# Kernel tuning notes

Hardware: AMD Instinct MI355X
Metric: run time of the kernel (lower is better)

The kernel has to match this reference:

```python
import jax, jax.numpy as jnp
import numpy as np

N_NODES = 20000
N_EDGES = 160000
N_GRAPHS = 100
IN_CH = 64
EDGE_DIM = 8
NEG_SLOPE = 0.2


def _gatv2(x, edge_index, edge_attr, Wl, Wr, We, att, b, heads, ch, n_nodes):
    # GATv2Conv: e_ij = att . leaky_relu(Wl x_j + Wr x_i [+ We e_ij]), softmax over dst i,
    # out_i = sum_j alpha_ij * (Wl x_j), concat heads, + bias.
    src, dst = edge_index[0], edge_index[1]
    xl = (x @ Wl).reshape(-1, heads, ch)  # [N,H,C] source-side transform
    xr = (x @ Wr).reshape(-1, heads, ch)  # [N,H,C] target-side transform
    m = xl[src] + xr[dst]                 # [E,H,C]
    if edge_attr is not None:
        m = m + (edge_attr @ We).reshape(-1, heads, ch)
    m = jax.nn.leaky_relu(m, NEG_SLOPE)
    logit = jnp.einsum('ehc,hc->eh', m, att)                     # [E,H]
    mx = jax.ops.segment_max(logit, dst, num_segments=n_nodes)   # [N,H]
    ex = jnp.exp(logit - mx[dst])
    den = jax.ops.segment_sum(ex, dst, num_segments=n_nodes)     # [N,H]
    alpha = ex / (den[dst] + 1e-16)                              # [E,H]
    out = jax.ops.segment_sum(alpha[:, :, None] * xl[src], dst, num_segments=n_nodes)
    return out.reshape(-1, heads * ch) + b


def setup_inputs() -> dict:
    key = jax.random.key(0)
    ks = jax.random.split(key, 24)
    def rn(k, shape, fan_in):
        return jax.random.normal(k, shape, dtype=jnp.float32) / np.sqrt(fan_in)
    inp = {}
    inp['x'] = jax.random.normal(ks[0], (N_NODES, IN_CH), dtype=jnp.float32)
    inp['edge_attr'] = jax.random.uniform(ks[1], (N_EDGES, EDGE_DIM), dtype=jnp.float32)
    inp['Wl1'] = rn(ks[2], (IN_CH, 1024), IN_CH)
    inp['Wr1'] = rn(ks[3], (IN_CH, 1024), IN_CH)
    inp['We1'] = rn(ks[4], (EDGE_DIM, 1024), EDGE_DIM)
    inp['att1'] = rn(ks[5], (4, 256), 256)
    inp['b1'] = jnp.zeros((1024,), jnp.float32)
    inp['Wl2'] = rn(ks[6], (1024, 256), 1024)
    inp['Wr2'] = rn(ks[7], (1024, 256), 1024)
    inp['We2'] = rn(ks[8], (EDGE_DIM, 256), EDGE_DIM)
    inp['att2'] = rn(ks[9], (4, 64), 64)
    inp['b2'] = jnp.zeros((256,), jnp.float32)
    inp['Wlp'] = rn(ks[10], (256, 384), 256)
    inp['Wrp'] = rn(ks[11], (256, 384), 256)
    inp['attp'] = rn(ks[12], (6, 64), 64)
    inp['bp'] = jnp.zeros((384,), jnp.float32)
    inp['Wfc1'] = rn(ks[13], (384, 64), 384)
    inp['bfc1'] = jnp.zeros((64,), jnp.float32)
    inp['Wfc2'] = rn(ks[14], (64, 1), 64)
    inp['bfc2'] = jnp.zeros((1,), jnp.float32)
    inp['edge_index'] = jax.random.randint(ks[15], (2, N_EDGES), 0, N_NODES, dtype=jnp.int32)
    inp['edge_index_master'] = jax.random.randint(ks[16], (2, N_EDGES), 0, N_NODES, dtype=jnp.int32)
    inp['n_nodes'] = jnp.full((N_GRAPHS,), N_NODES // N_GRAPHS, dtype=jnp.int32)
    return inp


def reference(x, edge_attr, Wl1, Wr1, We1, att1, b1, Wl2, Wr2, We2, att2, b2,
              Wlp, Wrp, attp, bp, Wfc1, bfc1, Wfc2, bfc2,
              edge_index, edge_index_master, n_nodes):
    h = _gatv2(x, edge_index, edge_attr, Wl1, Wr1, We1, att1, b1, 4, 256, N_NODES)
    h = jax.nn.relu(h)
    h = _gatv2(h, edge_index, edge_attr, Wl2, Wr2, We2, att2, b2, 4, 64, N_NODES)
    h = jax.nn.relu(h)
    h = _gatv2(h, edge_index_master, None, Wlp, Wrp, None, attp, bp, 6, 64, N_NODES)
    last_idx = jnp.cumsum(n_nodes) - 1          # master node = last node of each graph
    master = h[last_idx]                        # [G,384] (dropout p=0 -> identity)
    z = jax.nn.relu(master @ Wfc1 + bfc1)
    return z @ Wfc2 + bfc2                      # [G,1]
```

## Files before the change

kernel.cpp:

```cpp
#include <hip/hip_runtime.h>
#include <hip/hip_bf16.h>

#define DIV_UP(a,b) (((a)+(b)-1)/(b))

typedef __attribute__((ext_vector_type(8))) short short8;
typedef __attribute__((ext_vector_type(4))) float floatx4;

static __device__ __forceinline__ unsigned short f2bf(float v) {
    unsigned u = __builtin_bit_cast(unsigned, v);
    u += 0x7fffu + ((u >> 16) & 1u);
    return (unsigned short)(u >> 16);
}
static __device__ __forceinline__ float bflo(unsigned v) {
    return __builtin_bit_cast(float, v << 16);
}
static __device__ __forceinline__ float bfhi(unsigned v) {
    return __builtin_bit_cast(float, v & 0xffff0000u);
}

template <int CPL>
static __device__ __forceinline__ void load_bf16v(const unsigned short* p, float* d) {
    if constexpr (CPL == 8) {
        uint4 v = *(const uint4*)p;
        d[0] = bflo(v.x); d[1] = bfhi(v.x);
        d[2] = bflo(v.y); d[3] = bfhi(v.y);
        d[4] = bflo(v.z); d[5] = bfhi(v.z);
        d[6] = bflo(v.w); d[7] = bfhi(v.w);
    } else if constexpr (CPL == 4) {
        uint2 v = *(const uint2*)p;
        d[0] = bflo(v.x); d[1] = bfhi(v.x);
        d[2] = bflo(v.y); d[3] = bfhi(v.y);
    } else if constexpr (CPL == 2) {
        unsigned v = *(const unsigned*)p;
        d[0] = bflo(v); d[1] = bfhi(v);
    } else {
        d[0] = bflo(*p);
    }
}

template <int CPL>
static __device__ __forceinline__ void store_bf16v(unsigned short* p, const float* s) {
    unsigned short tmp[CPL];
#pragma unroll
    for (int c = 0; c < CPL; ++c) tmp[c] = f2bf(s[c]);
    if constexpr (CPL == 8) *(uint4*)p = *(uint4*)tmp;
    else if constexpr (CPL == 4) *(ushort4*)p = *(ushort4*)tmp;
    else if constexpr (CPL == 2) *(ushort2*)p = *(ushort2*)tmp;
    else p[0] = tmp[0];
}

template <int CTRL>
static __device__ __forceinline__ float dpp_mv(float x) {
    int r = __builtin_amdgcn_update_dpp(0, __builtin_bit_cast(int, x), CTRL, 0xF, 0xF, false);
    return __builtin_bit_cast(float, r);
}
template <int G>
static __device__ __forceinline__ float group_reduce(float x) {
    x += dpp_mv<0xB1>(x);
    x += dpp_mv<0x4E>(x);
    x += dpp_mv<0x124>(x);
    x += dpp_mv<0x128>(x);
    if constexpr (G >= 32) x += __shfl_xor(x, 16, 64);
    if constexpr (G >= 64) x += __shfl_xor(x, 32, 64);
    return x;
}

static __device__ __forceinline__ void tr_pair(const float* Wa, const float* Wb, int K, int Nn,
                                               unsigned short* Wt, int i) {
    int tot = K * Nn;
    const float* W = (i < tot) ? Wa : Wb;
    unsigned short* dst = Wt + ((i < tot) ? 0 : (size_t)Nn * K);
    int ii = (i < tot) ? i : i - tot;
    int k = ii % K, n = ii / K;
    dst[(size_t)n * K + k] = f2bf(W[(size_t)k * Nn + n]);
}

__global__ void prep_all(const float* __restrict__ x,
                         const float* __restrict__ Wl1, const float* __restrict__ Wr1,
                         const float* __restrict__ Wl2, const float* __restrict__ Wr2,
                         const float* __restrict__ Wlp, const float* __restrict__ Wrp,
                         unsigned short* __restrict__ xbf,
                         unsigned short* __restrict__ wt1, unsigned short* __restrict__ wt2,
                         unsigned short* __restrict__ wt3, int N) {
    const int S1 = 2 * 64 * 1024, S2 = 2 * 1024 * 256, S3 = 2 * 256 * 384;
    int id = blockIdx.x * blockDim.x + threadIdx.x;
    if (id < S1) tr_pair(Wl1, Wr1, 64, 1024, wt1, id);
    else if (id < S1 + S2) tr_pair(Wl2, Wr2, 1024, 256, wt2, id - S1);
    else if (id < S1 + S2 + S3) tr_pair(Wlp, Wrp, 256, 384, wt3, id - S1 - S2);
    else {
        int i = id - S1 - S2 - S3;
        if (i < N * 64) xbf[i] = f2bf(x[i]);
    }
}

__global__ __launch_bounds__(256) void gemm_mfma(
    const unsigned short* __restrict__ A, const unsigned short* __restrict__ Bt,
    unsigned short* __restrict__ C, int M, int Ntot, int K) {
    constexpr int LDA = 40;
    __shared__ unsigned short As[128 * LDA];
    __shared__ unsigned short Bs[128 * LDA];
    const int tid = threadIdx.x;
    const int m0 = blockIdx.y * 128, n0 = blockIdx.x * 128;
    const int wave = tid >> 6, lane = tid & 63;
    const int wm = (wave >> 1) * 64, wn = (wave & 1) * 64;
    const int r15 = lane & 15, quad = lane >> 4;
    const int sr = tid >> 1, skc = tid & 1;
    floatx4 acc[4][4];
#pragma unroll
    for (int i = 0; i < 4; ++i)
#pragma unroll
        for (int j = 0; j < 4; ++j) acc[i][j] = (floatx4)0.f;

    for (int k0 = 0; k0 < K; k0 += 32) {
        uint4 a0 = make_uint4(0, 0, 0, 0), a1 = make_uint4(0, 0, 0, 0);
        int am = m0 + sr;
        if (am < M) {
            const unsigned short* ap = A + (size_t)am * K + k0 + skc * 16;
            a0 = *(const uint4*)ap;
            a1 = *(const uint4*)(ap + 8);
        }
        const unsigned short* bp = Bt + (size_t)(n0 + sr) * K + k0 + skc * 16;
        uint4 b0 = *(const uint4*)bp;
        uint4 b1 = *(const uint4*)(bp + 8);
        *(uint4*)(&As[sr * LDA + skc * 16]) = a0;
        *(uint4*)(&As[sr * LDA + skc * 16 + 8]) = a1;
        *(uint4*)(&Bs[sr * LDA + skc * 16]) = b0;
        *(uint4*)(&Bs[sr * LDA + skc * 16 + 8]) = b1;
        __syncthreads();
        short8 af[4], bfr[4];
#pragma unroll
        for (int i = 0; i < 4; ++i)
            af[i] = *(const short8*)(&As[(wm + i * 16 + r15) * LDA + quad * 8]);
#pragma unroll
        for (int j = 0; j < 4; ++j)
            bfr[j] = *(const short8*)(&Bs[(wn + j * 16 + r15) * LDA + quad * 8]);
#pragma unroll
        for (int i = 0; i < 4; ++i)
#pragma unroll
            for (int j = 0; j < 4; ++j)
                acc[i][j] = __builtin_amdgcn_mfma_f32_16x16x32_bf16(af[i], bfr[j], acc[i][j], 0, 0, 0);
        __syncthreads();
    }
#pragma unroll
    for (int i = 0; i < 4; ++i)
#pragma unroll
        for (int j = 0; j < 4; ++j)
#pragma unroll
            for (int r = 0; r < 4; ++r) {
                int m = m0 + wm + i * 16 + quad * 4 + r;
                int n = n0 + wn + j * 16 + r15;
                if (m < M) C[(size_t)m * Ntot + n] = f2bf(acc[i][j][r]);
            }
}

__global__ void count2_kernel(const int* __restrict__ dst0, const int* __restrict__ dst1,
                              int E, int N, int* __restrict__ cnt) {
    int e = blockIdx.x * blockDim.x + threadIdx.x;
    if (e < E) atomicAdd(&cnt[dst0[e]], 1);
    else if (e < 2 * E) atomicAdd(&cnt[N + dst1[e - E]], 1);
}

__global__ __launch_bounds__(1024) void scan_kernel(const int* __restrict__ cnt_all, int N,
                                                    int* __restrict__ off_all, int* __restrict__ cur_all) {
    const int* cnt = cnt_all + blockIdx.x * N;
    int* off = off_all + blockIdx.x * (N + 1);
    int* cur = cur_all + blockIdx.x * N;
    __shared__ int part[1024];
    int t = threadIdx.x;
    int per = (N + 1023) >> 10;
    int base = t * per;
    int s = 0;
    for (int i = 0; i < per; ++i) { int idx = base + i; if (idx < N) s += cnt[idx]; }
    part[t] = s;
    __syncthreads();
    for (int d2 = 1; d2 < 1024; d2 <<= 1) {
        int v = (t >= d2) ? part[t - d2] : 0;
        __syncthreads();
        part[t] += v;
        __syncthreads();
    }
    int pre = (t == 0) ? 0 : part[t - 1];
    for (int i = 0; i < per; ++i) {
        int idx = base + i;
        if (idx < N) { off[idx] = pre; cur[idx] = pre; pre += cnt[idx]; }
    }
    if (t == 1023) off[N] = part[1023];
}

__global__ void fill2_kernel(const int* __restrict__ src0, const int* __restrict__ dst0,
                             const int* __restrict__ src1, const int* __restrict__ dst1,
                             int E, int N, int* __restrict__ cur, int2* __restrict__ edges) {
    int e = blockIdx.x * blockDim.x + threadIdx.x;
    if (e < E) {
        int p = atomicAdd(&cur[dst0[e]], 1);
        edges[p] = make_int2(src0[e], e);
    } else if (e < 2 * E) {
        int i = e - E;
        int p = atomicAdd(&cur[N + dst1[i]], 1);
        edges[E + p] = make_int2(src1[i], i);
    }
}

template <int D, int CPL, int QP, int G, int NE>
static __device__ __forceinline__ void hase_group(
    const unsigned short* __restrict__ xlr, const float* __restrict__ ea,
    const float* wb, const float (&att_r)[CPL], const float (&xr_r)[CPL],
    const int2* ep , int c0,
    float& m, float& l, float (&acc)[CPL]) {
    int2 e[NE];
#pragma unroll
    for (int n = 0; n < NE; ++n) e[n] = ep[n];
    float ev[NE][8];
#pragma unroll
    for (int n = 0; n < NE; ++n) {
        float4 a = ((const float4*)(ea + (size_t)e[n].y * 8))[0];
        float4 b = ((const float4*)(ea + (size_t)e[n].y * 8))[1];
        ev[n][0] = a.x; ev[n][1] = a.y; ev[n][2] = a.z; ev[n][3] = a.w;
        ev[n][4] = b.x; ev[n][5] = b.y; ev[n][6] = b.z; ev[n][7] = b.w;
    }
    float xv[NE][CPL], z[NE][CPL];
#pragma unroll
    for (int n = 0; n < NE; ++n) {
        load_bf16v<CPL>(xlr + (size_t)e[n].x * (2 * D) + c0, xv[n]);
#pragma unroll
        for (int c = 0; c < CPL; ++c) z[n][c] = xv[n][c] + xr_r[c];
    }
#pragma unroll
    for (int k = 0; k < 8; ++k) {
#pragma unroll
        for (int q = 0; q < CPL / 4; ++q) {
            float4 w4 = *(const float4*)(wb + k * D + q * QP);
#pragma unroll
            for (int n = 0; n < NE; ++n) {
                z[n][q * 4 + 0] = fmaf(ev[n][k], w4.x, z[n][q * 4 + 0]);
                z[n][q * 4 + 1] = fmaf(ev[n][k], w4.y, z[n][q * 4 + 1]);
                z[n][q * 4 + 2] = fmaf(ev[n][k], w4.z, z[n][q * 4 + 2]);
                z[n][q * 4 + 3] = fmaf(ev[n][k], w4.w, z[n][q * 4 + 3]);
            }
        }
    }
    float lg[NE];
#pragma unroll
    for (int n = 0; n < NE; ++n) {
        lg[n] = 0.f;
#pragma unroll
        for (int c = 0; c < CPL; ++c) {
            float a = z[n][c] > 0.f ? z[n][c] : 0.2f * z[n][c];
            lg[n] = fmaf(att_r[c], a, lg[n]);
        }
        lg[n] = group_reduce<G>(lg[n]);
    }
    float mn = m;
#pragma unroll
    for (int n = 0; n < NE; ++n) mn = fmaxf(mn, lg[n]);
    float sc = __expf(m - mn);
    float p[NE], ps = 0.f;
#pragma unroll
    for (int n = 0; n < NE; ++n) { p[n] = __expf(lg[n] - mn); ps += p[n]; }
    m = mn;
    l = fmaf(l, sc, ps);
#pragma unroll
    for (int c = 0; c < CPL; ++c) {
        float t = p[0] * xv[0][c];
#pragma unroll
        for (int n = 1; n < NE; ++n) t = fmaf(p[n], xv[n][c], t);
        acc[c] = fmaf(acc[c], sc, t);
    }
}

template <int D, int C, int CB, int WPN, bool RELU>
__global__ __launch_bounds__(256) void attn_hase(
    const unsigned short* __restrict__ xlr, const float* __restrict__ ea,
    const float* __restrict__ We, const float* __restrict__ att,
    const int2* __restrict__ edges, const int* __restrict__ off,
    const float* __restrict__ bias, unsigned short* __restrict__ outp, int N) {
    constexpr int CPL = CB / 64;
    constexpr int HW = CB / C;
    constexpr int G = 64 / HW;
    constexpr int NPB = 4 / WPN;
    constexpr int QP = CB * 4 / CPL;
    __shared__ float wsh[8 * D];
    for (int f4 = threadIdx.x; f4 < 2 * D; f4 += 256) {
        int k = f4 / (D / 4);
        int c = (f4 - k * (D / 4)) * 4;
        int b = c / CB, cc = c - b * CB;
        int ln = cc / CPL, q = (cc % CPL) / 4;
        int dst = k * (D / 4) + (b * CB + q * QP + ln * 4) / 4;
        ((float4*)wsh)[dst] = ((const float4*)We)[f4];
    }
    __syncthreads();

    const int wid = threadIdx.x >> 6, lane = threadIdx.x & 63;
    const int wv = wid % WPN, wn = wid / WPN;
    const int c0 = wv * CB + lane * CPL;
    const float* wb = wsh + wv * CB + lane * 4;

    float att_r[CPL];
#pragma unroll
    for (int c = 0; c < CPL; ++c) att_r[c] = att[c0 + c];

    for (int node = blockIdx.x * NPB + wn; node < N; node += gridDim.x * NPB) {
        float xr_r[CPL];
        load_bf16v<CPL>(xlr + (size_t)node * (2 * D) + D + c0, xr_r);
        float m = -1e30f, l = 0.f, acc[CPL];
#pragma unroll
        for (int c = 0; c < CPL; ++c) acc[c] = 0.f;

        const int jb = __builtin_amdgcn_readfirstlane(off[node]);
        const int je = __builtin_amdgcn_readfirstlane(off[node + 1]);
        int j = jb;
        for (; j + 4 <= je; j += 4)
            hase_group<D, CPL, QP, G, 4>(xlr, ea, wb, att_r, xr_r, edges + j, c0, m, l, acc);
        for (; j < je; ++j)
            hase_group<D, CPL, QP, G, 1>(xlr, ea, wb, att_r, xr_r, edges + j, c0, m, l, acc);

        float inv = 1.f / (l + 1e-16f);
        float r[CPL];
#pragma unroll
        for (int c = 0; c < CPL; ++c) {
            r[c] = fmaf(acc[c], inv, bias[c0 + c]);
            if constexpr (RELU) r[c] = fmaxf(r[c], 0.f);
        }
        store_bf16v<CPL>(outp + (size_t)node * D + c0, r);
    }
}

template <int D, int CPL, int G, int NE>
static __device__ __forceinline__ void noe_group(
    const unsigned short* __restrict__ xlr,
    const float (&att_r)[CPL], const float (&xr_r)[CPL],
    const int2* ep , int c0,
    float& m, float& l, float (&acc)[CPL]) {
    int2 e[NE];
#pragma unroll
    for (int n = 0; n < NE; ++n) e[n] = ep[n];
    float xv[NE][CPL], lg[NE];
#pragma unroll
    for (int n = 0; n < NE; ++n)
        load_bf16v<CPL>(xlr + (size_t)e[n].x * (2 * D) + c0, xv[n]);
#pragma unroll
    for (int n = 0; n < NE; ++n) {
        lg[n] = 0.f;
#pragma unroll
        for (int c = 0; c < CPL; ++c) {
            float z = xv[n][c] + xr_r[c];
            z = z > 0.f ? z : 0.2f * z;
            lg[n] = fmaf(att_r[c], z, lg[n]);
        }
        lg[n] = group_reduce<G>(lg[n]);
    }
    float mn = m;
#pragma unroll
    for (int n = 0; n < NE; ++n) mn = fmaxf(mn, lg[n]);
    float sc = __expf(m - mn);
    float p[NE], ps = 0.f;
#pragma unroll
    for (int n = 0; n < NE; ++n) { p[n] = __expf(lg[n] - mn); ps += p[n]; }
    m = mn;
    l = fmaf(l, sc, ps);
#pragma unroll
    for (int c = 0; c < CPL; ++c) {
        float t = p[0] * xv[0][c];
#pragma unroll
        for (int n = 1; n < NE; ++n) t = fmaf(p[n], xv[n][c], t);
        acc[c] = fmaf(acc[c], sc, t);
    }
}

template <int D, int C, int CB, bool RELU>
static __device__ __forceinline__ void attn_wave3(
    const unsigned short* __restrict__ xlr, const float* __restrict__ att,
    const int2* __restrict__ edges, int jb, int je,
    const float* __restrict__ bias, float* __restrict__ outp,
    int node, int cb, int lane) {
    constexpr int CPL = CB / 64;
    constexpr int HW = CB / C;
    constexpr int G = 64 / HW;
    const int c0 = cb + lane * CPL;

    float xr_r[CPL], att_r[CPL];
    load_bf16v<CPL>(xlr + (size_t)node * (2 * D) + D + c0, xr_r);
#pragma unroll
    for (int c = 0; c < CPL; ++c) att_r[c] = att[c0 + c];

    float m = -1e30f, l = 0.f, acc[CPL];
#pragma unroll
    for (int c = 0; c < CPL; ++c) acc[c] = 0.f;

    int j = jb;
    for (; j + 4 <= je; j += 4)
        noe_group<D, CPL, G, 4>(xlr, att_r, xr_r, edges + j, c0, m, l, acc);
    for (; j < je; ++j)
        noe_group<D, CPL, G, 1>(xlr, att_r, xr_r, edges + j, c0, m, l, acc);

    float inv = 1.f / (l + 1e-16f);
    float* out = outp + (size_t)node * D + c0;
    float tmp[CPL];
#pragma unroll
    for (int c = 0; c < CPL; ++c) {
        float r = fmaf(acc[c], inv, bias[c0 + c]);
        if constexpr (RELU) r = fmaxf(r, 0.f);
        tmp[c] = r;
    }
    if constexpr (CPL == 4) *(float4*)out = *(float4*)tmp;
    else if constexpr (CPL == 2) *(float2*)out = *(float2*)tmp;
    else out[0] = tmp[0];
}

template <int D, int C, int CB0, int CB1, bool RELU>
__global__ __launch_bounds__(256) void attn_noe(
    const unsigned short* __restrict__ xlr, const float* __restrict__ att,
    const int2* __restrict__ edges, const int* __restrict__ off,
    const float* __restrict__ bias, float* __restrict__ outp, int N) {
    const int wid = threadIdx.x >> 6, lane = threadIdx.x & 63;
    const int gw = blockIdx.x * 4 + wid;
    const int node = gw >> 1, wv = gw & 1;
    if (node >= N) return;
    const int jb = __builtin_amdgcn_readfirstlane(off[node]);
    const int je = __builtin_amdgcn_readfirstlane(off[node + 1]);
    if (wv == 0)
        attn_wave3<D, C, CB0, RELU>(xlr, att, edges, jb, je, bias, outp, node, 0, lane);
    else
        attn_wave3<D, C, CB1, RELU>(xlr, att, edges, jb, je, bias, outp, node, CB0, lane);
}

__global__ void mlp_kernel(const float* __restrict__ h3, const int* __restrict__ nn,
                           const float* __restrict__ Wfc1, const float* __restrict__ bfc1,
                           const float* __restrict__ Wfc2, const float* __restrict__ bfc2,
                           float* __restrict__ out, int G) {
    int g = blockIdx.x, t = threadIdx.x;
    int s = 0;
    for (int k = 0; k <= g; ++k) s += nn[k];
    const float* row = h3 + (size_t)(s - 1) * 384;
    float z = bfc1[t];
    for (int k = 0; k < 384; ++k) z = fmaf(row[k], Wfc1[k * 64 + t], z);
    z = fmaxf(z, 0.f);
    float v = z * Wfc2[t];
#pragma unroll
    for (int o = 32; o; o >>= 1) v += __shfl_xor(v, o, 64);
    if (t == 0) out[g] = v + bfc2[0];
}

extern "C" void kernel_launch(void* const* d_in, const int* in_sizes, int n_in,
                              void* d_out, int out_size, void* d_ws, size_t ws_size,
                              hipStream_t stream) {
    const float* x    = (const float*)d_in[0];
    const float* ea   = (const float*)d_in[1];
    const float* Wl1  = (const float*)d_in[2];
    const float* Wr1  = (const float*)d_in[3];
    const float* We1  = (const float*)d_in[4];
    const float* att1 = (const float*)d_in[5];
    const float* b1   = (const float*)d_in[6];
    const float* Wl2  = (const float*)d_in[7];
    const float* Wr2  = (const float*)d_in[8];
    const float* We2  = (const float*)d_in[9];
    const float* att2 = (const float*)d_in[10];
    const float* b2   = (const float*)d_in[11];
    const float* Wlp  = (const float*)d_in[12];
    const float* Wrp  = (const float*)d_in[13];
    const float* attp = (const float*)d_in[14];
    const float* bp   = (const float*)d_in[15];
    const float* Wfc1 = (const float*)d_in[16];
    const float* bfc1 = (const float*)d_in[17];
    const float* Wfc2 = (const float*)d_in[18];
    const float* bfc2 = (const float*)d_in[19];
    const int* ei     = (const int*)d_in[20];
    const int* eim    = (const int*)d_in[21];
    const int* nn     = (const int*)d_in[22];

    const int N = in_sizes[0] / 64;
    const int E = in_sizes[20] / 2;
    const int G = in_sizes[22];
    const int* src1 = ei,  *dst1 = ei + E;
    const int* srcm = eim, *dstm = eim + E;

    char* w = (char*)d_ws;
    size_t o = 0;
    auto alloc = [&](size_t b) { size_t r = o; o += (b + 255) & ~(size_t)255; return r; };
    char* R1 = w + alloc((size_t)N * 2048 * 2);
    unsigned short* xlr1 = (unsigned short*)R1;
    unsigned short* xlr3 = (unsigned short*)R1;
    float* h3 = (float*)(R1 + (size_t)N * 768 * 2 + 256);
    unsigned short* h1   = (unsigned short*)(w + alloc((size_t)N * 1024 * 2));
    unsigned short* xlr2 = (unsigned short*)(w + alloc((size_t)N * 512 * 2));
    unsigned short* h2   = (unsigned short*)(w + alloc((size_t)N * 256 * 2));
    unsigned short* xbf  = (unsigned short*)(w + alloc((size_t)N * 64 * 2));
    unsigned short* wt1  = (unsigned short*)(w + alloc((size_t)2048 * 64 * 2));
    unsigned short* wt2  = (unsigned short*)(w + alloc((size_t)512 * 1024 * 2));
    unsigned short* wt3  = (unsigned short*)(w + alloc((size_t)768 * 256 * 2));
    int*  cnt   = (int*)(w + alloc((size_t)2 * N * 4));
    int*  off   = (int*)(w + alloc((size_t)2 * (N + 1) * 4));
    int*  cur   = (int*)(w + alloc((size_t)2 * N * 4));
    int2* edges = (int2*)(w + alloc((size_t)2 * E * 8 + 4096));
    (void)ws_size; (void)n_in; (void)out_size;

    dim3 blk(256);

    {
        int tot = 2 * 64 * 1024 + 2 * 1024 * 256 + 2 * 256 * 384 + N * 64;
        prep_all<<<DIV_UP(tot, 256), blk, 0, stream>>>(x, Wl1, Wr1, Wl2, Wr2, Wlp, Wrp,
                                                       xbf, wt1, wt2, wt3, N);
    }

    hipMemsetAsync(cnt, 0, (size_t)2 * N * 4, stream);
    count2_kernel<<<DIV_UP(2 * E, 256), blk, 0, stream>>>(dst1, dstm, E, N, cnt);
    scan_kernel<<<2, 1024, 0, stream>>>(cnt, N, off, cur);
    fill2_kernel<<<DIV_UP(2 * E, 256), blk, 0, stream>>>(src1, dst1, srcm, dstm, E, N, cur, edges);
    const int* off3 = off + (N + 1);
    int2* edges3 = edges + E;

    gemm_mfma<<<dim3(2048 / 128, DIV_UP(N, 128)), blk, 0, stream>>>(xbf, wt1, xlr1, N, 2048, 64);
    attn_hase<1024, 256, 512, 2, true><<<2560, blk, 0, stream>>>(
        xlr1, ea, We1, att1, edges, off, b1, h1, N);

    gemm_mfma<<<dim3(512 / 128, DIV_UP(N, 128)), blk, 0, stream>>>(h1, wt2, xlr2, N, 512, 1024);
    attn_hase<256, 64, 256, 1, true><<<1280, blk, 0, stream>>>(
        xlr2, ea, We2, att2, edges, off, b2, h2, N);

    gemm_mfma<<<dim3(768 / 128, DIV_UP(N, 128)), blk, 0, stream>>>(h2, wt3, xlr3, N, 768, 256);
    attn_noe<384, 64, 256, 128, false><<<DIV_UP(N, 2), blk, 0, stream>>>(
        xlr3, attp, edges3, off3, bp, h3, N);

    mlp_kernel<<<G, 64, 0, stream>>>(h3, nn, Wfc1, bfc1, Wfc2, bfc2, (float*)d_out, G);
}
```

Before: 422.8 us.

## Direct-to-LDS GEMM loads, pre-gathered edge attributes, pipelined neighbor gathers, exp2 softmax

The MFMA GEMM now loads tiles with global_load_lds straight into unpadded LDS, which removes the register round-trip but drops the padding that avoided bank conflicts. A separate kernel writes edge attributes in CSR order, so the attention kernels read them contiguously instead of through edge-id indirection. A compact source-index array replaces the int2 edge records. The attention loops double-buffer the neighbor feature gathers so the next group's loads overlap the current group's compute. Softmax uses exp2 with log2(e) folded into the attention weights.

```diff
diff --git a/kernel.cpp b/kernel.cpp
--- a/kernel.cpp
+++ b/kernel.cpp
@@ -17,24 +17,28 @@
 static __device__ __forceinline__ float bfhi(unsigned v) {
     return __builtin_bit_cast(float, v & 0xffff0000u);
 }
+static __device__ __forceinline__ float fexp2(float x) { return __builtin_amdgcn_exp2f(x); }
+static __device__ __forceinline__ float f4get(const float4 v, int k) {
+    return k == 0 ? v.x : k == 1 ? v.y : k == 2 ? v.z : v.w;
+}
+
+template <int CPL> struct RawT;
+template <> struct RawT<8> { using T = uint4; };
+template <> struct RawT<4> { using T = uint2; };
+template <> struct RawT<2> { using T = unsigned; };
 
 template <int CPL>
-static __device__ __forceinline__ void load_bf16v(const unsigned short* p, float* d) {
+static __device__ __forceinline__ void unpackx(const typename RawT<CPL>::T& v, float* d) {
     if constexpr (CPL == 8) {
-        uint4 v = *(const uint4*)p;
         d[0] = bflo(v.x); d[1] = bfhi(v.x);
         d[2] = bflo(v.y); d[3] = bfhi(v.y);
         d[4] = bflo(v.z); d[5] = bfhi(v.z);
         d[6] = bflo(v.w); d[7] = bfhi(v.w);
     } else if constexpr (CPL == 4) {
-        uint2 v = *(const uint2*)p;
         d[0] = bflo(v.x); d[1] = bfhi(v.x);
         d[2] = bflo(v.y); d[3] = bfhi(v.y);
-    } else if constexpr (CPL == 2) {
-        unsigned v = *(const unsigned*)p;
+    } else {
         d[0] = bflo(v); d[1] = bfhi(v);
-    } else {
-        d[0] = bflo(*p);
     }
 }
 
@@ -93,18 +97,32 @@
     }
 }
 
+#define GLOAD_LDS16(gp, lp) \
+    __builtin_amdgcn_global_load_lds((const __attribute__((address_space(1))) void*)(gp), \
+                                     (__attribute__((address_space(3))) void*)(lp), 16, 0, 0)
+
 __global__ __launch_bounds__(256) void gemm_mfma(
     const unsigned short* __restrict__ A, const unsigned short* __restrict__ Bt,
     unsigned short* __restrict__ C, int M, int Ntot, int K) {
-    constexpr int LDA = 40;
-    __shared__ unsigned short As[128 * LDA];
-    __shared__ unsigned short Bs[128 * LDA];
+    __shared__ unsigned short As[128 * 32];
+    __shared__ unsigned short Bs[128 * 32];
     const int tid = threadIdx.x;
     const int m0 = blockIdx.y * 128, n0 = blockIdx.x * 128;
     const int wave = tid >> 6, lane = tid & 63;
     const int wm = (wave >> 1) * 64, wn = (wave & 1) * 64;
     const int r15 = lane & 15, quad = lane >> 4;
-    const int sr = tid >> 1, skc = tid & 1;
+    const int srow = lane >> 2, scol = (lane & 3) * 8;
+    const int arow0 = m0 + 32 * wave + srow;
+    const int brow0 = n0 + 32 * wave + srow;
+    const unsigned short* ap0 = A + (size_t)arow0 * K + scol;
+    const unsigned short* ap1 = ap0 + (size_t)16 * K;
+    const unsigned short* bp0 = Bt + (size_t)brow0 * K + scol;
+    const unsigned short* bp1 = bp0 + (size_t)16 * K;
+    unsigned short* alds0 = As + (32 * wave) * 32;
+    unsigned short* alds1 = alds0 + 16 * 32;
+    unsigned short* blds0 = Bs + (32 * wave) * 32;
+    unsigned short* blds1 = blds0 + 16 * 32;
+    const bool av0 = arow0 < M, av1 = (arow0 + 16) < M;
     floatx4 acc[4][4];
 #pragma unroll
     for (int i = 0; i < 4; ++i)
@@ -112,28 +130,19 @@
         for (int j = 0; j < 4; ++j) acc[i][j] = (floatx4)0.f;
 
     for (int k0 = 0; k0 < K; k0 += 32) {
-        uint4 a0 = make_uint4(0, 0, 0, 0), a1 = make_uint4(0, 0, 0, 0);
-        int am = m0 + sr;
-        if (am < M) {
-            const unsigned short* ap = A + (size_t)am * K + k0 + skc * 16;
-            a0 = *(const uint4*)ap;
-            a1 = *(const uint4*)(ap + 8);
-        }
-        const unsigned short* bp = Bt + (size_t)(n0 + sr) * K + k0 + skc * 16;
-        uint4 b0 = *(const uint4*)bp;
-        uint4 b1 = *(const uint4*)(bp + 8);
-        *(uint4*)(&As[sr * LDA + skc * 16]) = a0;
-        *(uint4*)(&As[sr * LDA + skc * 16 + 8]) = a1;
-        *(uint4*)(&Bs[sr * LDA + skc * 16]) = b0;
-        *(uint4*)(&Bs[sr * LDA + skc * 16 + 8]) = b1;
+        if (av0) GLOAD_LDS16(ap0, alds0);
+        if (av1) GLOAD_LDS16(ap1, alds1);
+        GLOAD_LDS16(bp0, blds0);
+        GLOAD_LDS16(bp1, blds1);
+        ap0 += 32; ap1 += 32; bp0 += 32; bp1 += 32;
         __syncthreads();
         short8 af[4], bfr[4];
 #pragma unroll
         for (int i = 0; i < 4; ++i)
-            af[i] = *(const short8*)(&As[(wm + i * 16 + r15) * LDA + quad * 8]);
+            af[i] = *(const short8*)(&As[(wm + i * 16 + r15) * 32 + quad * 8]);
 #pragma unroll
         for (int j = 0; j < 4; ++j)
-            bfr[j] = *(const short8*)(&Bs[(wn + j * 16 + r15) * LDA + quad * 8]);
+            bfr[j] = *(const short8*)(&Bs[(wn + j * 16 + r15) * 32 + quad * 8]);
 #pragma unroll
         for (int i = 0; i < 4; ++i)
 #pragma unroll
@@ -189,41 +198,67 @@
 
 __global__ void fill2_kernel(const int* __restrict__ src0, const int* __restrict__ dst0,
                              const int* __restrict__ src1, const int* __restrict__ dst1,
-                             int E, int N, int* __restrict__ cur, int2* __restrict__ edges) {
+                             int E, int N, int* __restrict__ cur, int2* __restrict__ edges,
+                             int* __restrict__ srcs) {
     int e = blockIdx.x * blockDim.x + threadIdx.x;
     if (e < E) {
         int p = atomicAdd(&cur[dst0[e]], 1);
         edges[p] = make_int2(src0[e], e);
+        srcs[p] = src0[e];
     } else if (e < 2 * E) {
         int i = e - E;
         int p = atomicAdd(&cur[N + dst1[i]], 1);
-        edges[E + p] = make_int2(src1[i], i);
-    }
+        srcs[E + p] = src1[i];
+    }
+}
+
+__global__ void ea_gather_kernel(const float* __restrict__ ea, const int2* __restrict__ edges,
+                                 float* __restrict__ ead, int E) {
+    int j = blockIdx.x * blockDim.x + threadIdx.x;
+    if (j >= E) return;
+    int ey = edges[j].y;
+    const float4* s = (const float4*)(ea + (size_t)ey * 8);
+    float4* o = (float4*)(ead + (size_t)j * 8);
+    o[0] = s[0];
+    o[1] = s[1];
+}
+
+template <int CPL, int NE>
+struct EStage {
+    int src[NE];
+    typename RawT<CPL>::T xv[NE];
+};
+
+template <int D, int CPL, int NE>
+static __device__ __forceinline__ void stage_x(
+    const unsigned short* __restrict__ xlr, const int* __restrict__ srcs,
+    int j, int c0, EStage<CPL, NE>& s) {
+#pragma unroll
+    for (int n = 0; n < NE; ++n) s.src[n] = srcs[j + n];
+#pragma unroll
+    for (int n = 0; n < NE; ++n)
+        s.xv[n] = *(const typename RawT<CPL>::T*)(xlr + (size_t)s.src[n] * (2 * D) + c0);
 }
 
 template <int D, int CPL, int QP, int G, int NE>
-static __device__ __forceinline__ void hase_group(
-    const unsigned short* __restrict__ xlr, const float* __restrict__ ea,
+static __device__ __forceinline__ void hase_compute(
+    const EStage<CPL, NE>& s, const float* __restrict__ ead, int j,
     const float* wb, const float (&att_r)[CPL], const float (&xr_r)[CPL],
-    const int2* ep , int c0,
     float& m, float& l, float (&acc)[CPL]) {
-    int2 e[NE];
-#pragma unroll
-    for (int n = 0; n < NE; ++n) e[n] = ep[n];
-    float ev[NE][8];
+    float4 evr[NE][2];
 #pragma unroll
     for (int n = 0; n < NE; ++n) {
-        float4 a = ((const float4*)(ea + (size_t)e[n].y * 8))[0];
-        float4 b = ((const float4*)(ea + (size_t)e[n].y * 8))[1];
-        ev[n][0] = a.x; ev[n][1] = a.y; ev[n][2] = a.z; ev[n][3] = a.w;
-        ev[n][4] = b.x; ev[n][5] = b.y; ev[n][6] = b.z; ev[n][7] = b.w;
-    }
-    float xv[NE][CPL], z[NE][CPL];
+        const float4* q = (const float4*)(ead + (size_t)(j + n) * 8);
+        evr[n][0] = q[0];
+        evr[n][1] = q[1];
+    }
+    float z[NE][CPL];
 #pragma unroll
     for (int n = 0; n < NE; ++n) {
-        load_bf16v<CPL>(xlr + (size_t)e[n].x * (2 * D) + c0, xv[n]);
-#pragma unroll
-        for (int c = 0; c < CPL; ++c) z[n][c] = xv[n][c] + xr_r[c];
+        float xv[CPL];
+        unpackx<CPL>(s.xv[n], xv);
+#pragma unroll
+        for (int c = 0; c < CPL; ++c) z[n][c] = xv[c] + xr_r[c];
     }
 #pragma unroll
     for (int k = 0; k < 8; ++k) {
@@ -232,47 +267,50 @@
             float4 w4 = *(const float4*)(wb + k * D + q * QP);
 #pragma unroll
             for (int n = 0; n < NE; ++n) {
-                z[n][q * 4 + 0] = fmaf(ev[n][k], w4.x, z[n][q * 4 + 0]);
-                z[n][q * 4 + 1] = fmaf(ev[n][k], w4.y, z[n][q * 4 + 1]);
-                z[n][q * 4 + 2] = fmaf(ev[n][k], w4.z, z[n][q * 4 + 2]);
-                z[n][q * 4 + 3] = fmaf(ev[n][k], w4.w, z[n][q * 4 + 3]);
+                float ek = f4get(evr[n][k >> 2], k & 3);
+                z[n][q * 4 + 0] = fmaf(ek, w4.x, z[n][q * 4 + 0]);
+                z[n][q * 4 + 1] = fmaf(ek, w4.y, z[n][q * 4 + 1]);
+                z[n][q * 4 + 2] = fmaf(ek, w4.z, z[n][q * 4 + 2]);
+                z[n][q * 4 + 3] = fmaf(ek, w4.w, z[n][q * 4 + 3]);
             }
         }
     }
     float lg[NE];
 #pragma unroll
     for (int n = 0; n < NE; ++n) {
-        lg[n] = 0.f;
+        float t = 0.f;
 #pragma unroll
         for (int c = 0; c < CPL; ++c) {
             float a = z[n][c] > 0.f ? z[n][c] : 0.2f * z[n][c];
-            lg[n] = fmaf(att_r[c], a, lg[n]);
-        }
-        lg[n] = group_reduce<G>(lg[n]);
+            t = fmaf(att_r[c], a, t);
+        }
+        lg[n] = group_reduce<G>(t);
     }
     float mn = m;
 #pragma unroll
     for (int n = 0; n < NE; ++n) mn = fmaxf(mn, lg[n]);
-    float sc = __expf(m - mn);
+    float sc = fexp2(m - mn);
     float p[NE], ps = 0.f;
 #pragma unroll
-    for (int n = 0; n < NE; ++n) { p[n] = __expf(lg[n] - mn); ps += p[n]; }
+    for (int n = 0; n < NE; ++n) { p[n] = fexp2(lg[n] - mn); ps += p[n]; }
     m = mn;
     l = fmaf(l, sc, ps);
 #pragma unroll
-    for (int c = 0; c < CPL; ++c) {
-        float t = p[0] * xv[0][c];
-#pragma unroll
-        for (int n = 1; n < NE; ++n) t = fmaf(p[n], xv[n][c], t);
-        acc[c] = fmaf(acc[c], sc, t);
+    for (int c = 0; c < CPL; ++c) acc[c] *= sc;
+#pragma unroll
+    for (int n = 0; n < NE; ++n) {
+        float xv[CPL];
+        unpackx<CPL>(s.xv[n], xv);
+#pragma unroll
+        for (int c = 0; c < CPL; ++c) acc[c] = fmaf(p[n], xv[c], acc[c]);
     }
 }
 
 template <int D, int C, int CB, int WPN, bool RELU>
 __global__ __launch_bounds__(256) void attn_hase(
-    const unsigned short* __restrict__ xlr, const float* __restrict__ ea,
+    const unsigned short* __restrict__ xlr, const float* __restrict__ ead,
     const float* __restrict__ We, const float* __restrict__ att,
-    const int2* __restrict__ edges, const int* __restrict__ off,
+    const int* __restrict__ srcs, const int* __restrict__ off,
     const float* __restrict__ bias, unsigned short* __restrict__ outp, int N) {
     constexpr int CPL = CB / 64;
     constexpr int HW = CB / C;
@@ -295,13 +333,16 @@
     const int c0 = wv * CB + lane * CPL;
     const float* wb = wsh + wv * CB + lane * 4;
 
+    const float L2E = 1.4426950408889634f;
     float att_r[CPL];
 #pragma unroll
-    for (int c = 0; c < CPL; ++c) att_r[c] = att[c0 + c];
+    for (int c = 0; c < CPL; ++c) att_r[c] = att[c0 + c] * L2E;
 
     for (int node = blockIdx.x * NPB + wn; node < N; node += gridDim.x * NPB) {
+        typename RawT<CPL>::T xrw =
+            *(const typename RawT<CPL>::T*)(xlr + (size_t)node * (2 * D) + D + c0);
         float xr_r[CPL];
-        load_bf16v<CPL>(xlr + (size_t)node * (2 * D) + D + c0, xr_r);
+        unpackx<CPL>(xrw, xr_r);
         float m = -1e30f, l = 0.f, acc[CPL];
 #pragma unroll
         for (int c = 0; c < CPL; ++c) acc[c] = 0.f;
@@ -309,10 +350,33 @@
         const int jb = __builtin_amdgcn_readfirstlane(off[node]);
         const int je = __builtin_amdgcn_readfirstlane(off[node + 1]);
         int j = jb;
-        for (; j + 4 <= je; j += 4)
-            hase_group<D, CPL, QP, G, 4>(xlr, ea, wb, att_r, xr_r, edges + j, c0, m, l, acc);
-        for (; j < je; ++j)
-            hase_group<D, CPL, QP, G, 1>(xlr, ea, wb, att_r, xr_r, edges + j, c0, m, l, acc);
+        int g = (je - jb) >> 2;
+        if (g > 0) {
+            EStage<CPL, 4> A, B;
+            stage_x<D, CPL, 4>(xlr, srcs, j, c0, A);
+            while (g >= 2) {
+                stage_x<D, CPL, 4>(xlr, srcs, j + 4, c0, B);
+                hase_compute<D, CPL, QP, G, 4>(A, ead, j, wb, att_r, xr_r, m, l, acc);
+                j += 4; --g;
+                if (g >= 2) {
+                    stage_x<D, CPL, 4>(xlr, srcs, j + 4, c0, A);
+                    hase_compute<D, CPL, QP, G, 4>(B, ead, j, wb, att_r, xr_r, m, l, acc);
+                    j += 4; --g;
+                } else if (g == 1) {
+                    hase_compute<D, CPL, QP, G, 4>(B, ead, j, wb, att_r, xr_r, m, l, acc);
+                    j += 4; --g;
+                }
+            }
+            if (g == 1) {
+                hase_compute<D, CPL, QP, G, 4>(A, ead, j, wb, att_r, xr_r, m, l, acc);
+                j += 4;
+            }
+        }
+        for (; j < je; ++j) {
+            EStage<CPL, 1> S;
+            stage_x<D, CPL, 1>(xlr, srcs, j, c0, S);
+            hase_compute<D, CPL, QP, G, 1>(S, ead, j, wb, att_r, xr_r, m, l, acc);
+        }
 
         float inv = 1.f / (l + 1e-16f);
         float r[CPL];
@@ -326,36 +390,31 @@
 }
 
 template <int D, int CPL, int G, int NE>
-static __device__ __forceinline__ void noe_group(
-    const unsigned short* __restrict__ xlr,
+static __device__ __forceinline__ void noe_compute(
+    const EStage<CPL, NE>& s,
     const float (&att_r)[CPL], const float (&xr_r)[CPL],
-    const int2* ep , int c0,
     float& m, float& l, float (&acc)[CPL]) {
-    int2 e[NE];
-#pragma unroll
-    for (int n = 0; n < NE; ++n) e[n] = ep[n];
     float xv[NE][CPL], lg[NE];
 #pragma unroll
-    for (int n = 0; n < NE; ++n)
-        load_bf16v<CPL>(xlr + (size_t)e[n].x * (2 * D) + c0, xv[n]);
+    for (int n = 0; n < NE; ++n) unpackx<CPL>(s.xv[n], xv[n]);
 #pragma unroll
     for (int n = 0; n < NE; ++n) {
-        lg[n] = 0.f;
+        float t = 0.f;
 #pragma unroll
         for (int c = 0; c < CPL; ++c) {
             float z = xv[n][c] + xr_r[c];
             z = z > 0.f ? z : 0.2f * z;
-            lg[n] = fmaf(att_r[c], z, lg[n]);
-        }
-        lg[n] = group_reduce<G>(lg[n]);
+            t = fmaf(att_r[c], z, t);
+        }
+        lg[n] = group_reduce<G>(t);
     }
     float mn = m;
 #pragma unroll
     for (int n = 0; n < NE; ++n) mn = fmaxf(mn, lg[n]);
-    float sc = __expf(m - mn);
+    float sc = fexp2(m - mn);
     float p[NE], ps = 0.f;
 #pragma unroll
-    for (int n = 0; n < NE; ++n) { p[n] = __expf(lg[n] - mn); ps += p[n]; }
+    for (int n = 0; n < NE; ++n) { p[n] = fexp2(lg[n] - mn); ps += p[n]; }
     m = mn;
     l = fmaf(l, sc, ps);
 #pragma unroll
@@ -370,28 +429,54 @@
 template <int D, int C, int CB, bool RELU>
 static __device__ __forceinline__ void attn_wave3(
     const unsigned short* __restrict__ xlr, const float* __restrict__ att,
-    const int2* __restrict__ edges, int jb, int je,
+    const int* __restrict__ srcs, int jb, int je,
     const float* __restrict__ bias, float* __restrict__ outp,
     int node, int cb, int lane) {
     constexpr int CPL = CB / 64;
     constexpr int HW = CB / C;
     constexpr int G = 64 / HW;
     const int c0 = cb + lane * CPL;
-
+    const float L2E = 1.4426950408889634f;
+
+    typename RawT<CPL>::T xrw =
+        *(const typename RawT<CPL>::T*)(xlr + (size_t)node * (2 * D) + D + c0);
     float xr_r[CPL], att_r[CPL];
-    load_bf16v<CPL>(xlr + (size_t)node * (2 * D) + D + c0, xr_r);
-#pragma unroll
-    for (int c = 0; c < CPL; ++c) att_r[c] = att[c0 + c];
+    unpackx<CPL>(xrw, xr_r);
+#pragma unroll
+    for (int c = 0; c < CPL; ++c) att_r[c] = att[c0 + c] * L2E;
 
     float m = -1e30f, l = 0.f, acc[CPL];
 #pragma unroll
     for (int c = 0; c < CPL; ++c) acc[c] = 0.f;
 
     int j = jb;
-    for (; j + 4 <= je; j += 4)
-        noe_group<D, CPL, G, 4>(xlr, att_r, xr_r, edges + j, c0, m, l, acc);
-    for (; j < je; ++j)
-        noe_group<D, CPL, G, 1>(xlr, att_r, xr_r, edges + j, c0, m, l, acc);
+    int g = (je - jb) >> 2;
+    if (g > 0) {
+        EStage<CPL, 4> A, B;
+        stage_x<D, CPL, 4>(xlr, srcs, j, c0, A);
+        while (g >= 2) {
+            stage_x<D, CPL, 4>(xlr, srcs, j + 4, c0, B);
+            noe_compute<D, CPL, G, 4>(A, att_r, xr_r, m, l, acc);
+            j += 4; --g;
+            if (g >= 2) {
+                stage_x<D, CPL, 4>(xlr, srcs, j + 4, c0, A);
+                noe_compute<D, CPL, G, 4>(B, att_r, xr_r, m, l, acc);
+                j += 4; --g;
+            } else if (g == 1) {
+                noe_compute<D, CPL, G, 4>(B, att_r, xr_r, m, l, acc);
+                j += 4; --g;
+            }
+        }
+        if (g == 1) {
+            noe_compute<D, CPL, G, 4>(A, att_r, xr_r, m, l, acc);
+            j += 4;
+        }
+    }
+    for (; j < je; ++j) {
+        EStage<CPL, 1> S;
+        stage_x<D, CPL, 1>(xlr, srcs, j, c0, S);
+        noe_compute<D, CPL, G, 1>(S, att_r, xr_r, m, l, acc);
+    }
 
     float inv = 1.f / (l + 1e-16f);
     float* out = outp + (size_t)node * D + c0;
@@ -410,7 +495,7 @@
 template <int D, int C, int CB0, int CB1, bool RELU>
 __global__ __launch_bounds__(256) void attn_noe(
     const unsigned short* __restrict__ xlr, const float* __restrict__ att,
-    const int2* __restrict__ edges, const int* __restrict__ off,
+    const int* __restrict__ srcs, const int* __restrict__ off,
     const float* __restrict__ bias, float* __restrict__ outp, int N) {
     const int wid = threadIdx.x >> 6, lane = threadIdx.x & 63;
     const int gw = blockIdx.x * 4 + wid;
@@ -419,9 +504,9 @@
     const int jb = __builtin_amdgcn_readfirstlane(off[node]);
     const int je = __builtin_amdgcn_readfirstlane(off[node + 1]);
     if (wv == 0)
-        attn_wave3<D, C, CB0, RELU>(xlr, att, edges, jb, je, bias, outp, node, 0, lane);
+        attn_wave3<D, C, CB0, RELU>(xlr, att, srcs, jb, je, bias, outp, node, 0, lane);
     else
-        attn_wave3<D, C, CB1, RELU>(xlr, att, edges, jb, je, bias, outp, node, CB0, lane);
+        attn_wave3<D, C, CB1, RELU>(xlr, att, srcs, jb, je, bias, outp, node, CB0, lane);
 }
 
 __global__ void mlp_kernel(const float* __restrict__ h3, const int* __restrict__ nn,
@@ -491,8 +576,13 @@
     int*  cnt   = (int*)(w + alloc((size_t)2 * N * 4));
     int*  off   = (int*)(w + alloc((size_t)2 * (N + 1) * 4));
     int*  cur   = (int*)(w + alloc((size_t)2 * N * 4));
-    int2* edges = (int2*)(w + alloc((size_t)2 * E * 8 + 4096));
+    char* eReg  = w + alloc((size_t)2 * E * 8 + 4096);
+    int2* edges = (int2*)eReg;
+    int*  srcs  = (int*)(eReg + (size_t)E * 8);
     (void)ws_size; (void)n_in; (void)out_size;
+
+    float* ead1 = (float*)xlr2;
+    float* ead2 = (float*)h1;
 
     dim3 blk(256);
 
@@ -505,21 +595,24 @@
     hipMemsetAsync(cnt, 0, (size_t)2 * N * 4, stream);
     count2_kernel<<<DIV_UP(2 * E, 256), blk, 0, stream>>>(dst1, dstm, E, N, cnt);
     scan_kernel<<<2, 1024, 0, stream>>>(cnt, N, off, cur);
-    fill2_kernel<<<DIV_UP(2 * E, 256), blk, 0, stream>>>(src1, dst1, srcm, dstm, E, N, cur, edges);
+    fill2_kernel<<<DIV_UP(2 * E, 256), blk, 0, stream>>>(src1, dst1, srcm, dstm, E, N, cur,
+                                                         edges, srcs);
+    ea_gather_kernel<<<DIV_UP(E, 256), blk, 0, stream>>>(ea, edges, ead1, E);
     const int* off3 = off + (N + 1);
-    int2* edges3 = edges + E;
+    const int* srcs3 = srcs + E;
 
     gemm_mfma<<<dim3(2048 / 128, DIV_UP(N, 128)), blk, 0, stream>>>(xbf, wt1, xlr1, N, 2048, 64);
     attn_hase<1024, 256, 512, 2, true><<<2560, blk, 0, stream>>>(
-        xlr1, ea, We1, att1, edges, off, b1, h1, N);
+        xlr1, ead1, We1, att1, srcs, off, b1, h1, N);
 
     gemm_mfma<<<dim3(512 / 128, DIV_UP(N, 128)), blk, 0, stream>>>(h1, wt2, xlr2, N, 512, 1024);
+    ea_gather_kernel<<<DIV_UP(E, 256), blk, 0, stream>>>(ea, edges, ead2, E);
     attn_hase<256, 64, 256, 1, true><<<1280, blk, 0, stream>>>(
-        xlr2, ea, We2, att2, edges, off, b2, h2, N);
+        xlr2, ead2, We2, att2, srcs, off, b2, h2, N);
 
     gemm_mfma<<<dim3(768 / 128, DIV_UP(N, 128)), blk, 0, stream>>>(h2, wt3, xlr3, N, 768, 256);
     attn_noe<384, 64, 256, 128, false><<<DIV_UP(N, 2), blk, 0, stream>>>(
-        xlr3, attp, edges3, off3, bp, h3, N);
+        xlr3, attp, srcs3, off3, bp, h3, N);
 
     mlp_kernel<<<G, 64, 0, stream>>>(h3, nn, Wfc1, bfc1, Wfc2, bfc2, (float*)d_out, G);
 }
```

New measurement: 456.1 us. 1.08x slower.
